# Optimization experiments

Measured on AMD Instinct MI355X. Metric: run time of the kernel, lower is better.

The kernel has to match this reference:

```python
import jax, jax.numpy as jnp
import numpy as np

D_MODEL = 768
N_HEADS = 12
NUM_EXPERTS = 4
TOP_K = 2
SPAN_LEN = 64
GATE_HIDDEN = 128


def setup_inputs() -> dict:
    key = jax.random.key(0)
    ks = jax.random.split(key, 14)
    B, T, C, E = 4, 4096, D_MODEL, NUM_EXPERTS
    s = 0.02
    return {
        "hidden_states": jax.random.normal(ks[0], (B, T, C), jnp.float32),
        "Wq": jax.random.normal(ks[1], (E, C, C), jnp.float32) * s,
        "bq": jnp.zeros((E, C), jnp.float32),
        "Wk": jax.random.normal(ks[2], (E, C, C), jnp.float32) * s,
        "bk": jnp.zeros((E, C), jnp.float32),
        "Wv": jax.random.normal(ks[3], (E, C, C), jnp.float32) * s,
        "bv": jnp.zeros((E, C), jnp.float32),
        "gW1": jax.random.normal(ks[4], (GATE_HIDDEN, C), jnp.float32) * s,
        "gb1": jnp.zeros((GATE_HIDDEN,), jnp.float32),
        "gW2": jax.random.normal(ks[5], (E, GATE_HIDDEN), jnp.float32) * s,
        "gb2": jnp.zeros((E,), jnp.float32),
        "Wo": jax.random.normal(ks[6], (C, C), jnp.float32) * s,
        "bo": jnp.zeros((C,), jnp.float32),
    }


def _moe_proj(w, x, W, b):
    # per-expert projection then gate-weighted sum over experts
    # x: (B,N,S,C), W: (E,O,C), w: (B,N,E)
    proj = jnp.einsum("bnsc,eoc->ebnso", x, W)          # (E,B,N,S,C)
    out = jnp.einsum("bne,ebnso->bnso", w, proj)
    out = out + jnp.einsum("bne,eo->bno", w, b)[:, :, None, :]
    return out


def reference(hidden_states, Wq, bq, Wk, bk, Wv, bv, gW1, gb1, gW2, gb2, Wo, bo):
    B, T, C = hidden_states.shape
    S, H, E, K = SPAN_LEN, N_HEADS, NUM_EXPERTS, TOP_K
    Dh = C // H
    N = T // S  # T is a multiple of span_len -> no padding, all-ones masks
    x = hidden_states.reshape(B, N, S, C)

    # gating: mean-pool per span -> MLP -> top-k softmax scattered to E slots
    pooled = x.mean(axis=2)                                  # (B,N,C)
    h = jax.nn.relu(pooled @ gW1.T + gb1)
    logits = h @ gW2.T + gb2                                 # (B,N,E)
    vals, idx = jax.lax.top_k(logits, K)
    sm = jax.nn.softmax(vals, axis=-1)                       # (B,N,K)
    w = jnp.sum(jax.nn.one_hot(idx, E, dtype=sm.dtype) * sm[..., None], axis=-2)  # (B,N,E)
    entropy = -jnp.mean(jnp.sum(w * jnp.log(jnp.clip(w, 1e-9)), axis=-1))

    # gate-weighted expert QKV projections
    q = _moe_proj(w, x, Wq, bq).reshape(B, N, S, H, Dh)
    k = _moe_proj(w, x, Wk, bk).reshape(B, N, S, H, Dh)
    v = _moe_proj(w, x, Wv, bv).reshape(B, N, S, H, Dh)

    # per-span attention (mask is all ones; dropout in eval mode)
    scores = jnp.einsum("bnshd,bnthd->bnhst", q, k) / jnp.sqrt(jnp.float32(Dh))
    attn = jax.nn.softmax(scores, axis=-1)
    out = jnp.einsum("bnhst,bnthd->bnshd", attn, v).reshape(B, T, C)
    out = out @ Wo.T + bo
    return out, entropy
```

## Files before the change

### kernel.cpp

```cpp
#include <hip/hip_runtime.h>
#include <hip/hip_bf16.h>
#include <hip/hip_fp16.h>

typedef _Float16 f16;
typedef _Float16 f16x8 __attribute__((ext_vector_type(8)));
typedef _Float16 f16x4 __attribute__((ext_vector_type(4)));
typedef float f32x4 __attribute__((ext_vector_type(4)));

constexpr int B = 4;
constexpr int T = 4096;
constexpr int C = 768;
constexpr int NH = 12;
constexpr int DH = 64;
constexpr int E = 4;
constexpr int SPAN = 64;
constexpr int N = T / SPAN;
constexpr int BN = B * N;
constexpr int GH = 128;
constexpr int BTC = B * T * C;

constexpr int U_X  = BTC / 8;
constexpr int U_WE = E * C * C / 8;
constexpr int U_WO = C * C / 8;
constexpr int U_TOT = U_X + 3 * U_WE + U_WO;

__global__ void cvt_all(const float* __restrict__ x,
                        const float* __restrict__ Wq, const float* __restrict__ Wk,
                        const float* __restrict__ Wv, const float* __restrict__ Wo,
                        f16* __restrict__ x16,
                        f16* __restrict__ Wq16, f16* __restrict__ Wk16,
                        f16* __restrict__ Wv16, f16* __restrict__ Wo16) {
    int i = blockIdx.x * blockDim.x + threadIdx.x;
    int stride = gridDim.x * blockDim.x;
    for (; i < U_TOT; i += stride) {
        const float* src; f16* dst; int u;
        if (i < U_X)                { src = x;  dst = x16;  u = i; }
        else if (i < U_X + U_WE)    { src = Wq; dst = Wq16; u = i - U_X; }
        else if (i < U_X + 2*U_WE)  { src = Wk; dst = Wk16; u = i - U_X - U_WE; }
        else if (i < U_X + 3*U_WE)  { src = Wv; dst = Wv16; u = i - U_X - 2*U_WE; }
        else                        { src = Wo; dst = Wo16; u = i - U_X - 3*U_WE; }
        float4 a = ((const float4*)src)[2 * u];
        float4 b = ((const float4*)src)[2 * u + 1];
        f16x8 o;
        o[0] = (f16)a.x; o[1] = (f16)a.y; o[2] = (f16)a.z; o[3] = (f16)a.w;
        o[4] = (f16)b.x; o[5] = (f16)b.y; o[6] = (f16)b.z; o[7] = (f16)b.w;
        ((f16x8*)dst)[u] = o;
    }
}

__global__ void gate_kernel(const float* __restrict__ x,
                            const float* __restrict__ gW1, const float* __restrict__ gb1,
                            const float* __restrict__ gW2, const float* __restrict__ gb2,
                            int* __restrict__ eidx, float* __restrict__ ewts,
                            float* __restrict__ ent_partial) {
    int span = blockIdx.x;
    int tid = threadIdx.x;
    __shared__ float pooled[C];
    __shared__ float h[GH];
    __shared__ float logits[E];

    const float* xb = x + (size_t)span * SPAN * C;
    for (int c = tid; c < C; c += 256) {
        float s = 0.f;
        #pragma unroll 8
        for (int t = 0; t < SPAN; ++t) s += xb[t * C + c];
        pooled[c] = s * (1.f / 64.f);
    }
    __syncthreads();

    if (tid < GH) {
        float acc = gb1[tid];
        const float* wrow = gW1 + (size_t)tid * C;
        #pragma unroll 8
        for (int c = 0; c < C; ++c) acc += pooled[c] * wrow[c];
        h[tid] = acc > 0.f ? acc : 0.f;
    }
    __syncthreads();

    if (tid < E) {
        float acc = gb2[tid];
        const float* wrow = gW2 + (size_t)tid * GH;
        #pragma unroll 8
        for (int j = 0; j < GH; ++j) acc += h[j] * wrow[j];
        logits[tid] = acc;
    }
    __syncthreads();

    if (tid == 0) {
        int i0 = 0; float v0 = logits[0];
        for (int e = 1; e < E; ++e) { if (logits[e] > v0) { v0 = logits[e]; i0 = e; } }
        int i1 = -1; float v1 = -3.0e38f;
        for (int e = 0; e < E; ++e) { if (e != i0 && logits[e] > v1) { v1 = logits[e]; i1 = e; } }
        float bq_ = expf(v1 - v0);
        float s = 1.f + bq_;
        float sm0 = 1.f / s;
        float sm1 = bq_ / s;
        eidx[span * 2 + 0] = i0;
        eidx[span * 2 + 1] = i1;
        ewts[span * 2 + 0] = sm0;
        ewts[span * 2 + 1] = sm1;
        float p0 = fmaxf(sm0, 1e-9f), p1 = fmaxf(sm1, 1e-9f);
        ent_partial[span] = sm0 * logf(p0) + sm1 * logf(p1);
    }
}

__global__ void entropy_kernel(const float* __restrict__ ent_partial, float* __restrict__ out_ent) {
    __shared__ float sh[256];
    int tid = threadIdx.x;
    sh[tid] = ent_partial[tid];
    __syncthreads();
    for (int s = 128; s > 0; s >>= 1) {
        if (tid < s) sh[tid] += sh[tid + s];
        __syncthreads();
    }
    if (tid == 0) *out_ent = -sh[0] * (1.0f / (float)BN);
}

__global__ __launch_bounds__(256) void qkv_mfma(
    const f16* __restrict__ xh,
    const f16* __restrict__ Wq16, const float* __restrict__ bq,
    const f16* __restrict__ Wk16, const float* __restrict__ bk,
    const f16* __restrict__ Wv16, const float* __restrict__ bv,
    const int* __restrict__ eidx, const float* __restrict__ ewts,
    f16* __restrict__ q16, f16* __restrict__ k16, f16* __restrict__ vt)
{
    int span  = blockIdx.x;
    int otile = blockIdx.y;
    int proj  = blockIdx.z;

    const f16* W; const float* bias; f16* out;
    if (proj == 0)      { W = Wq16; bias = bq; out = q16; }
    else if (proj == 1) { W = Wk16; bias = bk; out = k16; }
    else                { W = Wv16; bias = bv; out = vt; }

    int e0 = eidx[span * 2 + 0], e1 = eidx[span * 2 + 1];
    float w0 = ewts[span * 2 + 0], w1 = ewts[span * 2 + 1];
    f16 w0h = (f16)w0, w1h = (f16)w1;

    __shared__ f16x8 xs_u[64 * 8];
    __shared__ f16x8 ws_u[256 * 8];

    const f16x8* xu  = (const f16x8*)(xh + (size_t)span * 64 * C);
    const f16x8* Wu0 = (const f16x8*)(W + ((size_t)e0 * C + otile * 256) * (size_t)C);
    const f16x8* Wu1 = (const f16x8*)(W + ((size_t)e1 * C + otile * 256) * (size_t)C);

    int tid = threadIdx.x;
    int lane = tid & 63, wv = tid >> 6;
    int lr = lane & 15, lg = lane >> 4;

    f32x4 acc[4][4] = {};

    f16x8 xr[2], w0r[8], w1r[8];
    #pragma unroll
    for (int i = 0; i < 2; ++i) {
        int id = tid + i * 256;
        xr[i] = xu[(id >> 3) * 96 + (id & 7)];
    }
    #pragma unroll
    for (int i = 0; i < 8; ++i) {
        int id = tid + i * 256;
        w0r[i] = Wu0[(size_t)(id >> 3) * 96 + (id & 7)];
        w1r[i] = Wu1[(size_t)(id >> 3) * 96 + (id & 7)];
    }

    for (int kc8 = 0; kc8 < 96; kc8 += 8) {
        #pragma unroll
        for (int i = 0; i < 2; ++i) {
            int id = tid + i * 256;
            int r = id >> 3, u = id & 7;
            xs_u[r * 8 + (u ^ (r & 7))] = xr[i];
        }
        #pragma unroll
        for (int i = 0; i < 8; ++i) {
            int id = tid + i * 256;
            int r = id >> 3, u = id & 7;
            ws_u[r * 8 + (u ^ (r & 7))] = w0r[i] * w0h + w1r[i] * w1h;
        }

        if (kc8 < 88) {
            int kn = kc8 + 8;
            #pragma unroll
            for (int i = 0; i < 2; ++i) {
                int id = tid + i * 256;
                xr[i] = xu[(id >> 3) * 96 + kn + (id & 7)];
            }
            #pragma unroll
            for (int i = 0; i < 8; ++i) {
                int id = tid + i * 256;
                w0r[i] = Wu0[(size_t)(id >> 3) * 96 + kn + (id & 7)];
                w1r[i] = Wu1[(size_t)(id >> 3) * 96 + kn + (id & 7)];
            }
        }

        asm volatile("s_waitcnt lgkmcnt(0)" ::: "memory");
        __builtin_amdgcn_s_barrier();
        __builtin_amdgcn_sched_barrier(0);

        #pragma unroll
        for (int kk = 0; kk < 2; ++kk) {
            int ub = kk * 4 + lg;
            f16x8 afrag[4], bfrag[4];
            #pragma unroll
            for (int m = 0; m < 4; ++m) {
                int r = m * 16 + lr;
                afrag[m] = xs_u[r * 8 + (ub ^ (r & 7))];
            }
            #pragma unroll
            for (int n = 0; n < 4; ++n) {
                int r = wv * 64 + n * 16 + lr;
                bfrag[n] = ws_u[r * 8 + (ub ^ (r & 7))];
            }
            #pragma unroll
            for (int m = 0; m < 4; ++m)
                #pragma unroll
                for (int n = 0; n < 4; ++n)
                    acc[m][n] = __builtin_amdgcn_mfma_f32_16x16x32_f16(afrag[m], bfrag[n], acc[m][n], 0, 0, 0);
        }

        asm volatile("s_waitcnt lgkmcnt(0)" ::: "memory");
        __builtin_amdgcn_s_barrier();
        __builtin_amdgcn_sched_barrier(0);
    }

    if (proj == 2) {
        f16* vtb = out + (size_t)span * C * 64;
        #pragma unroll
        for (int n = 0; n < 4; ++n) {
            int col = otile * 256 + wv * 64 + n * 16 + lr;
            float be = w0 * bias[(size_t)e0 * C + col] + w1 * bias[(size_t)e1 * C + col];
            #pragma unroll
            for (int m = 0; m < 4; ++m) {
                f16x4 pk;
                #pragma unroll
                for (int r = 0; r < 4; ++r) pk[r] = (f16)(acc[m][n][r] + be);
                *(f16x4*)&vtb[(size_t)col * 64 + m * 16 + lg * 4] = pk;
            }
        }
    } else {
        f16* outb = out + (size_t)span * 64 * C;
        #pragma unroll
        for (int n = 0; n < 4; ++n) {
            int col = otile * 256 + wv * 64 + n * 16 + lr;
            float be = w0 * bias[(size_t)e0 * C + col] + w1 * bias[(size_t)e1 * C + col];
            #pragma unroll
            for (int m = 0; m < 4; ++m) {
                #pragma unroll
                for (int r = 0; r < 4; ++r) {
                    int row = m * 16 + lg * 4 + r;
                    outb[(size_t)row * C + col] = (f16)(acc[m][n][r] + be);
                }
            }
        }
    }
}

__global__ __launch_bounds__(256) void attn_mfma(
    const f16* __restrict__ q16, const f16* __restrict__ k16,
    const f16* __restrict__ vt, f16* __restrict__ a16)
{
    int h = blockIdx.x, span = blockIdx.y;
    __shared__ __align__(16) f16 Klds[64 * 72];
    __shared__ __align__(16) f16 Vlds[64 * 72];
    __shared__ __align__(16) f16 Plds[64 * 72];

    int tid = threadIdx.x;
    int lane = tid & 63, mt = tid >> 6;
    int lr = lane & 15, lg = lane >> 4;

    const f16x8* ku = (const f16x8*)k16;
    const f16x8* vu = (const f16x8*)vt;
    #pragma unroll
    for (int i = 0; i < 2; ++i) {
        int id = tid + i * 256;
        int r = id >> 3, u = id & 7;
        *(f16x8*)&Klds[r * 72 + u * 8] = ku[(size_t)span * 6144 + (size_t)r * 96 + h * 8 + u];
        *(f16x8*)&Vlds[r * 72 + u * 8] = vu[(size_t)span * 6144 + (size_t)(h * 64 + r) * 8 + u];
    }
    __syncthreads();

    const f16x8* qu = (const f16x8*)q16;
    f16x8 qa[2];
    #pragma unroll
    for (int kk = 0; kk < 2; ++kk)
        qa[kk] = qu[(size_t)span * 6144 + (size_t)(mt * 16 + lr) * 96 + h * 8 + kk * 4 + lg];

    f32x4 accs[4] = {};
    #pragma unroll
    for (int nt = 0; nt < 4; ++nt) {
        #pragma unroll
        for (int kk = 0; kk < 2; ++kk) {
            f16x8 kb = *(const f16x8*)&Klds[(nt * 16 + lr) * 72 + kk * 32 + lg * 8];
            accs[nt] = __builtin_amdgcn_mfma_f32_16x16x32_f16(qa[kk], kb, accs[nt], 0, 0, 0);
        }
    }

    #pragma unroll
    for (int nt = 0; nt < 4; ++nt) accs[nt] *= 0.125f;
    f32x4 m4;
    #pragma unroll
    for (int r = 0; r < 4; ++r)
        m4[r] = fmaxf(fmaxf(accs[0][r], accs[1][r]), fmaxf(accs[2][r], accs[3][r]));
    #pragma unroll
    for (int st = 1; st < 16; st <<= 1) {
        #pragma unroll
        for (int r = 0; r < 4; ++r) m4[r] = fmaxf(m4[r], __shfl_xor(m4[r], st));
    }
    f32x4 ps[4];
    f32x4 sum4 = {0.f, 0.f, 0.f, 0.f};
    #pragma unroll
    for (int nt = 0; nt < 4; ++nt)
        #pragma unroll
        for (int r = 0; r < 4; ++r) {
            ps[nt][r] = __expf(accs[nt][r] - m4[r]);
            sum4[r] += ps[nt][r];
        }
    #pragma unroll
    for (int st = 1; st < 16; st <<= 1) {
        #pragma unroll
        for (int r = 0; r < 4; ++r) sum4[r] += __shfl_xor(sum4[r], st);
    }
    f32x4 inv4;
    #pragma unroll
    for (int r = 0; r < 4; ++r) inv4[r] = 1.0f / sum4[r];

    #pragma unroll
    for (int nt = 0; nt < 4; ++nt)
        #pragma unroll
        for (int r = 0; r < 4; ++r)
            Plds[(mt * 16 + lg * 4 + r) * 72 + nt * 16 + lr] = (f16)ps[nt][r];
    __syncthreads();

    f16x8 pa[2];
    #pragma unroll
    for (int kkt = 0; kkt < 2; ++kkt)
        pa[kkt] = *(const f16x8*)&Plds[(mt * 16 + lr) * 72 + kkt * 32 + lg * 8];
    f32x4 acco[4] = {};
    #pragma unroll
    for (int nt = 0; nt < 4; ++nt) {
        #pragma unroll
        for (int kkt = 0; kkt < 2; ++kkt) {
            f16x8 vb = *(const f16x8*)&Vlds[(nt * 16 + lr) * 72 + kkt * 32 + lg * 8];
            acco[nt] = __builtin_amdgcn_mfma_f32_16x16x32_f16(pa[kkt], vb, acco[nt], 0, 0, 0);
        }
    }

    #pragma unroll
    for (int nt = 0; nt < 4; ++nt)
        #pragma unroll
        for (int r = 0; r < 4; ++r)
            Klds[(mt * 16 + lg * 4 + r) * 72 + nt * 16 + lr] = (f16)(acco[nt][r] * inv4[r]);
    __syncthreads();

    int row = mt * 16 + (lane >> 2);
    int u2 = (lane & 3) * 2;
    f16x8 o0 = *(const f16x8*)&Klds[row * 72 + u2 * 8];
    f16x8 o1 = *(const f16x8*)&Klds[row * 72 + u2 * 8 + 8];
    f16x8* au = (f16x8*)a16;
    au[(size_t)span * 6144 + (size_t)row * 96 + h * 8 + u2]     = o0;
    au[(size_t)span * 6144 + (size_t)row * 96 + h * 8 + u2 + 1] = o1;
}

__global__ __launch_bounds__(512) void outproj_mfma(
    const f16* __restrict__ ah, const f16* __restrict__ Wo16,
    const float* __restrict__ bo, float* __restrict__ Y)
{
    int rt = blockIdx.x;
    int otile = blockIdx.y;

    __shared__ f16x8 as_u[128 * 8];
    __shared__ f16x8 ws_u[256 * 8];

    const f16x8* au  = (const f16x8*)(ah + (size_t)rt * 128 * C);
    const f16x8* Wou = (const f16x8*)(Wo16 + (size_t)otile * 256 * C);

    int tid = threadIdx.x;
    int lane = tid & 63, wv = tid >> 6;
    int lr = lane & 15, lg = lane >> 4;
    int wm = (wv >> 2) * 64;
    int wn = (wv & 3) * 64;

    f32x4 acc[4][4] = {};

    for (int kc8 = 0; kc8 < 96; kc8 += 8) {
        #pragma unroll
        for (int i = 0; i < 2; ++i) {
            int id = tid + i * 512;
            int r = id >> 3, u = id & 7;
            as_u[r * 8 + (u ^ (r & 7))] = au[(size_t)r * 96 + kc8 + u];
        }
        #pragma unroll
        for (int i = 0; i < 4; ++i) {
            int id = tid + i * 512;
            int r = id >> 3, u = id & 7;
            ws_u[r * 8 + (u ^ (r & 7))] = Wou[(size_t)r * 96 + kc8 + u];
        }
        __syncthreads();
        #pragma unroll
        for (int kk = 0; kk < 2; ++kk) {
            int ub = kk * 4 + lg;
            f16x8 afrag[4], bfrag[4];
            #pragma unroll
            for (int m = 0; m < 4; ++m) {
                int r = wm + m * 16 + lr;
                afrag[m] = as_u[r * 8 + (ub ^ (r & 7))];
            }
            #pragma unroll
            for (int n = 0; n < 4; ++n) {
                int r = wn + n * 16 + lr;
                bfrag[n] = ws_u[r * 8 + (ub ^ (r & 7))];
            }
            #pragma unroll
            for (int m = 0; m < 4; ++m)
                #pragma unroll
                for (int n = 0; n < 4; ++n)
                    acc[m][n] = __builtin_amdgcn_mfma_f32_16x16x32_f16(afrag[m], bfrag[n], acc[m][n], 0, 0, 0);
        }
        __syncthreads();
    }

    #pragma unroll
    for (int n = 0; n < 4; ++n) {
        int col = otile * 256 + wn + n * 16 + lr;
        float be = bo[col];
        #pragma unroll
        for (int m = 0; m < 4; ++m) {
            #pragma unroll
            for (int r = 0; r < 4; ++r) {
                int row = rt * 128 + wm + m * 16 + lg * 4 + r;
                Y[(size_t)row * C + col] = acc[m][n][r] + be;
            }
        }
    }
}

extern "C" void kernel_launch(void* const* d_in, const int* in_sizes, int n_in,
                              void* d_out, int out_size, void* d_ws, size_t ws_size,
                              hipStream_t stream) {
    const float* x   = (const float*)d_in[0];
    const float* Wq  = (const float*)d_in[1];
    const float* bq  = (const float*)d_in[2];
    const float* Wk  = (const float*)d_in[3];
    const float* bk  = (const float*)d_in[4];
    const float* Wv  = (const float*)d_in[5];
    const float* bv  = (const float*)d_in[6];
    const float* gW1 = (const float*)d_in[7];
    const float* gb1 = (const float*)d_in[8];
    const float* gW2 = (const float*)d_in[9];
    const float* gb2 = (const float*)d_in[10];
    const float* Wo  = (const float*)d_in[11];
    const float* bo  = (const float*)d_in[12];

    float* out = (float*)d_out;

    char* ws = (char*)d_ws;
    const size_t h_btc = (size_t)BTC * sizeof(f16);
    f16* x16  = (f16*)(ws);
    f16* q16  = (f16*)(ws + 1 * h_btc);
    f16* k16  = (f16*)(ws + 2 * h_btc);
    f16* vt16 = (f16*)(ws + 3 * h_btc);
    f16* a16  = (f16*)(ws + 4 * h_btc);
    size_t off = 5 * h_btc;
    const size_t wsz = (size_t)E * C * C * sizeof(f16);
    f16* Wq16 = (f16*)(ws + off); off += wsz;
    f16* Wk16 = (f16*)(ws + off); off += wsz;
    f16* Wv16 = (f16*)(ws + off); off += wsz;
    f16* Wo16 = (f16*)(ws + off); off += (size_t)C * C * sizeof(f16);
    int*   eidx = (int*)(ws + off); off += 2048;
    float* ewts = (float*)(ws + off); off += 2048;
    float* entp = (float*)(ws + off);

    cvt_all<<<dim3(2048), dim3(256), 0, stream>>>(x, Wq, Wk, Wv, Wo,
                                                  x16, Wq16, Wk16, Wv16, Wo16);

    gate_kernel<<<dim3(BN), dim3(256), 0, stream>>>(x, gW1, gb1, gW2, gb2, eidx, ewts, entp);
    entropy_kernel<<<dim3(1), dim3(256), 0, stream>>>(entp, out + BTC);

    qkv_mfma<<<dim3(BN, 3, 3), dim3(256), 0, stream>>>(x16, Wq16, bq, Wk16, bk, Wv16, bv,
                                                       eidx, ewts, q16, k16, vt16);
    attn_mfma<<<dim3(NH, BN), dim3(256), 0, stream>>>(q16, k16, vt16, a16);
    outproj_mfma<<<dim3(128, 3), dim3(512), 0, stream>>>(a16, Wo16, bo, out);
}
```

Measured before the change: 218.9 us.

## Fuse x conversion with span pooling and split weight prefetch in QKV loop

```diff
diff --git a/kernel.cpp b/kernel.cpp
--- a/kernel.cpp
+++ b/kernel.cpp
@@ -19,26 +19,54 @@
 constexpr int GH = 128;
 constexpr int BTC = B * T * C;
 
-constexpr int U_X  = BTC / 8;
 constexpr int U_WE = E * C * C / 8;
 constexpr int U_WO = C * C / 8;
-constexpr int U_TOT = U_X + 3 * U_WE + U_WO;
-
-__global__ void cvt_all(const float* __restrict__ x,
-                        const float* __restrict__ Wq, const float* __restrict__ Wk,
-                        const float* __restrict__ Wv, const float* __restrict__ Wo,
-                        f16* __restrict__ x16,
-                        f16* __restrict__ Wq16, f16* __restrict__ Wk16,
-                        f16* __restrict__ Wv16, f16* __restrict__ Wo16) {
+constexpr int U_WTOT = 3 * U_WE + U_WO;
+
+__global__ __launch_bounds__(768) void cvt_x_pool(
+    const float* __restrict__ x, f16* __restrict__ x16,
+    float* __restrict__ pooled) {
+    int span = blockIdx.x;
+    int tid = threadIdx.x;
+    int u = tid % 96, rg = tid / 96;
+    __shared__ float part[8][C];
+
+    const float* xb = x + (size_t)span * SPAN * C;
+    f16* xo = x16 + (size_t)span * SPAN * C;
+    float a8[8] = {};
+    #pragma unroll
+    for (int j = 0; j < 8; ++j) {
+        int r = rg * 8 + j;
+        const float4* s = (const float4*)(xb + (size_t)r * C + u * 8);
+        float4 A = s[0], Bv = s[1];
+        f16x8 o;
+        o[0] = (f16)A.x;  o[1] = (f16)A.y;  o[2] = (f16)A.z;  o[3] = (f16)A.w;
+        o[4] = (f16)Bv.x; o[5] = (f16)Bv.y; o[6] = (f16)Bv.z; o[7] = (f16)Bv.w;
+        *(f16x8*)(xo + (size_t)r * C + u * 8) = o;
+        a8[0] += A.x;  a8[1] += A.y;  a8[2] += A.z;  a8[3] += A.w;
+        a8[4] += Bv.x; a8[5] += Bv.y; a8[6] += Bv.z; a8[7] += Bv.w;
+    }
+    #pragma unroll
+    for (int j = 0; j < 8; ++j) part[rg][u * 8 + j] = a8[j];
+    __syncthreads();
+    float s = 0.f;
+    #pragma unroll
+    for (int g = 0; g < 8; ++g) s += part[g][tid];
+    pooled[(size_t)span * C + tid] = s * (1.f / 64.f);
+}
+
+__global__ void cvt_w(const float* __restrict__ Wq, const float* __restrict__ Wk,
+                      const float* __restrict__ Wv, const float* __restrict__ Wo,
+                      f16* __restrict__ Wq16, f16* __restrict__ Wk16,
+                      f16* __restrict__ Wv16, f16* __restrict__ Wo16) {
     int i = blockIdx.x * blockDim.x + threadIdx.x;
     int stride = gridDim.x * blockDim.x;
-    for (; i < U_TOT; i += stride) {
+    for (; i < U_WTOT; i += stride) {
         const float* src; f16* dst; int u;
-        if (i < U_X)                { src = x;  dst = x16;  u = i; }
-        else if (i < U_X + U_WE)    { src = Wq; dst = Wq16; u = i - U_X; }
-        else if (i < U_X + 2*U_WE)  { src = Wk; dst = Wk16; u = i - U_X - U_WE; }
-        else if (i < U_X + 3*U_WE)  { src = Wv; dst = Wv16; u = i - U_X - 2*U_WE; }
-        else                        { src = Wo; dst = Wo16; u = i - U_X - 3*U_WE; }
+        if (i < U_WE)               { src = Wq; dst = Wq16; u = i; }
+        else if (i < 2 * U_WE)      { src = Wk; dst = Wk16; u = i - U_WE; }
+        else if (i < 3 * U_WE)      { src = Wv; dst = Wv16; u = i - 2 * U_WE; }
+        else                        { src = Wo; dst = Wo16; u = i - 3 * U_WE; }
         float4 a = ((const float4*)src)[2 * u];
         float4 b = ((const float4*)src)[2 * u + 1];
         f16x8 o;
@@ -48,31 +76,26 @@
     }
 }
 
-__global__ void gate_kernel(const float* __restrict__ x,
-                            const float* __restrict__ gW1, const float* __restrict__ gb1,
-                            const float* __restrict__ gW2, const float* __restrict__ gb2,
-                            int* __restrict__ eidx, float* __restrict__ ewts,
-                            float* __restrict__ ent_partial) {
+__global__ __launch_bounds__(128) void gate_mlp(
+    const float* __restrict__ pooled,
+    const float* __restrict__ gW1, const float* __restrict__ gb1,
+    const float* __restrict__ gW2, const float* __restrict__ gb2,
+    int* __restrict__ eidx, float* __restrict__ ewts,
+    float* __restrict__ ent_partial) {
     int span = blockIdx.x;
     int tid = threadIdx.x;
-    __shared__ float pooled[C];
+    __shared__ float pl[C];
     __shared__ float h[GH];
     __shared__ float logits[E];
 
-    const float* xb = x + (size_t)span * SPAN * C;
-    for (int c = tid; c < C; c += 256) {
-        float s = 0.f;
-        #pragma unroll 8
-        for (int t = 0; t < SPAN; ++t) s += xb[t * C + c];
-        pooled[c] = s * (1.f / 64.f);
-    }
-    __syncthreads();
-
-    if (tid < GH) {
+    for (int c = tid; c < C; c += 128) pl[c] = pooled[(size_t)span * C + c];
+    __syncthreads();
+
+    {
         float acc = gb1[tid];
         const float* wrow = gW1 + (size_t)tid * C;
         #pragma unroll 8
-        for (int c = 0; c < C; ++c) acc += pooled[c] * wrow[c];
+        for (int c = 0; c < C; ++c) acc += pl[c] * wrow[c];
         h[tid] = acc > 0.f ? acc : 0.f;
     }
     __syncthreads();
@@ -185,7 +208,7 @@
                 xr[i] = xu[(id >> 3) * 96 + kn + (id & 7)];
             }
             #pragma unroll
-            for (int i = 0; i < 8; ++i) {
+            for (int i = 0; i < 4; ++i) {
                 int id = tid + i * 256;
                 w0r[i] = Wu0[(size_t)(id >> 3) * 96 + kn + (id & 7)];
                 w1r[i] = Wu1[(size_t)(id >> 3) * 96 + kn + (id & 7)];
@@ -196,9 +219,40 @@
         __builtin_amdgcn_s_barrier();
         __builtin_amdgcn_sched_barrier(0);
 
-        #pragma unroll
-        for (int kk = 0; kk < 2; ++kk) {
-            int ub = kk * 4 + lg;
+        {
+            int ub = lg;
+            f16x8 afrag[4], bfrag[4];
+            #pragma unroll
+            for (int m = 0; m < 4; ++m) {
+                int r = m * 16 + lr;
+                afrag[m] = xs_u[r * 8 + (ub ^ (r & 7))];
+            }
+            #pragma unroll
+            for (int n = 0; n < 4; ++n) {
+                int r = wv * 64 + n * 16 + lr;
+                bfrag[n] = ws_u[r * 8 + (ub ^ (r & 7))];
+            }
+            #pragma unroll
+            for (int m = 0; m < 4; ++m)
+                #pragma unroll
+                for (int n = 0; n < 4; ++n)
+                    acc[m][n] = __builtin_amdgcn_mfma_f32_16x16x32_f16(afrag[m], bfrag[n], acc[m][n], 0, 0, 0);
+        }
+
+        __builtin_amdgcn_sched_barrier(0);
+        if (kc8 < 88) {
+            int kn = kc8 + 8;
+            #pragma unroll
+            for (int i = 4; i < 8; ++i) {
+                int id = tid + i * 256;
+                w0r[i] = Wu0[(size_t)(id >> 3) * 96 + kn + (id & 7)];
+                w1r[i] = Wu1[(size_t)(id >> 3) * 96 + kn + (id & 7)];
+            }
+        }
+        __builtin_amdgcn_sched_barrier(0);
+
+        {
+            int ub = 4 + lg;
             f16x8 afrag[4], bfrag[4];
             #pragma unroll
             for (int m = 0; m < 4; ++m) {
@@ -467,12 +521,14 @@
     f16* Wo16 = (f16*)(ws + off); off += (size_t)C * C * sizeof(f16);
     int*   eidx = (int*)(ws + off); off += 2048;
     float* ewts = (float*)(ws + off); off += 2048;
-    float* entp = (float*)(ws + off);
-
-    cvt_all<<<dim3(2048), dim3(256), 0, stream>>>(x, Wq, Wk, Wv, Wo,
-                                                  x16, Wq16, Wk16, Wv16, Wo16);
-
-    gate_kernel<<<dim3(BN), dim3(256), 0, stream>>>(x, gW1, gb1, gW2, gb2, eidx, ewts, entp);
+    float* entp = (float*)(ws + off); off += 1024;
+    float* pooled = (float*)(ws + off); off += (size_t)BN * C * sizeof(float);
+
+    cvt_x_pool<<<dim3(BN), dim3(768), 0, stream>>>(x, x16, pooled);
+    cvt_w<<<dim3(1024), dim3(256), 0, stream>>>(Wq, Wk, Wv, Wo,
+                                                Wq16, Wk16, Wv16, Wo16);
+    gate_mlp<<<dim3(BN), dim3(128), 0, stream>>>(pooled, gW1, gb1, gW2, gb2,
+                                                 eidx, ewts, entp);
     entropy_kernel<<<dim3(1), dim3(256), 0, stream>>>(entp, out + BTC);
 
     qkv_mfma<<<dim3(BN, 3, 3), dim3(256), 0, stream>>>(x16, Wq16, bq, Wk16, bk, Wv16, bv,
```

Result: no change. 215.9 us (-1.4%).
